# Optimization experiments

Hardware: AMD Instinct MI355X
Metric: run time of the kernel (lower is better)

The kernel has to match this reference:

```python
import jax, jax.numpy as jnp
import numpy as np

N, D, K = 262144, 64, 512


def setup_inputs() -> dict:
    key = jax.random.key(0)
    k1, k2 = jax.random.split(key)
    x = jax.random.normal(k1, (N, D), dtype=jnp.float32)
    # embedding initialized uniform(-1/K, 1/K) as in the torch module
    codebook = jax.random.uniform(k2, (K, D), dtype=jnp.float32, minval=-1.0 / K, maxval=1.0 / K)
    return {"x": x, "codebook": codebook}


def reference(x, codebook):
    # distances[n,k] = ||x_n||^2 + ||w_k||^2 - 2 x_n . w_k  (cdist^2 via matmul)
    d = (jnp.sum(x * x, axis=1, keepdims=True)
         + jnp.sum(codebook * codebook, axis=1)
         - 2.0 * jnp.matmul(x, codebook.T))  # [N, K]
    indices = jnp.argmin(d, axis=1)          # [N]
    x_q = codebook[indices]                  # [N, D] gather
    commitment_loss = jnp.mean((jax.lax.stop_gradient(x_q) - x) ** 2)
    embedding_loss = jnp.mean((x_q - jax.lax.stop_gradient(x)) ** 2)
    vq_loss = commitment_loss * 0.25 + embedding_loss
    # straight-through estimator
    x_out = x + jax.lax.stop_gradient(x_q - x)
    return (x_out, vq_loss)
```

## Files before the change

kernel.cpp:

```cpp
#include <hip/hip_runtime.h>
#include <hip/hip_bf16.h>

#define N_ROWS 262144
#define DIM    64
#define KCB    512

#define BLOCKS  512
#define THREADS 512

typedef __bf16 bf16x8 __attribute__((ext_vector_type(8)));
typedef float  f32x4  __attribute__((ext_vector_type(4)));

__device__ inline float dot4(float4 a) {
    return a.x * a.x + a.y * a.y + a.z * a.z + a.w * a.w;
}
__device__ inline unsigned umin2(unsigned a, unsigned b) { return a < b ? a : b; }

__device__ inline void conv_col(float4 f0, float4 f1, float4 f2, float4 f3,
                                bf16x8& lo, bf16x8& hi, float& xn) {
    xn = dot4(f0) + dot4(f1) + dot4(f2) + dot4(f3);
    lo[0] = (__bf16)f0.x; lo[1] = (__bf16)f0.y; lo[2] = (__bf16)f0.z; lo[3] = (__bf16)f0.w;
    lo[4] = (__bf16)f1.x; lo[5] = (__bf16)f1.y; lo[6] = (__bf16)f1.z; lo[7] = (__bf16)f1.w;
    hi[0] = (__bf16)f2.x; hi[1] = (__bf16)f2.y; hi[2] = (__bf16)f2.z; hi[3] = (__bf16)f2.w;
    hi[4] = (__bf16)f3.x; hi[5] = (__bf16)f3.y; hi[6] = (__bf16)f3.z; hi[7] = (__bf16)f3.w;
}

__global__ __launch_bounds__(THREADS, 2) void vq_main(
    const float* __restrict__ x, const float* __restrict__ cb,
    float* __restrict__ out, float* __restrict__ partials)
{
    __shared__ bf16x8 cb_sh[KCB * 8];
    __shared__ f32x4  wn_sh4[KCB / 4];
    __shared__ float  red_sh[8];

    const int tid    = threadIdx.x;
    const int lane   = tid & 63;
    const int wave   = tid >> 6;
    const int lane15 = lane & 15;
    const int half   = lane >> 4;

    const int wrow = blockIdx.x * 512 + wave * 64;
    const float* xc0 = x + (size_t)(wrow + lane15) * DIM + half * 8;
    const float* xc1 = x + (size_t)(wrow + 16 + lane15) * DIM + half * 8;

    float4 p00 = *(const float4*)xc0,        p01 = *(const float4*)(xc0 + 4);
    float4 p02 = *(const float4*)(xc0 + 32), p03 = *(const float4*)(xc0 + 36);
    float4 p10 = *(const float4*)xc1,        p11 = *(const float4*)(xc1 + 4);
    float4 p12 = *(const float4*)(xc1 + 32), p13 = *(const float4*)(xc1 + 36);

    #pragma unroll
    for (int it = 0; it < (KCB * 8) / THREADS; ++it) {
        const int fg = tid + it * THREADS;
        const int row = fg >> 3, g = fg & 7;
        const float* src = cb + row * DIM + g * 8;
        float4 f0 = *(const float4*)src;
        float4 f1 = *(const float4*)(src + 4);
        float sq = dot4(f0) + dot4(f1);
        sq += __shfl_xor(sq, 1);
        sq += __shfl_xor(sq, 2);
        sq += __shfl_xor(sq, 4);
        bf16x8 v;
        v[0] = (__bf16)(-f0.x); v[1] = (__bf16)(-f0.y); v[2] = (__bf16)(-f0.z); v[3] = (__bf16)(-f0.w);
        v[4] = (__bf16)(-f1.x); v[5] = (__bf16)(-f1.y); v[6] = (__bf16)(-f1.z); v[7] = (__bf16)(-f1.w);
        cb_sh[row * 8 + (g ^ (row & 7))] = v;
        if (g == 0) ((float*)wn_sh4)[row] = 1.0f + 0.5f * sq;
    }

    bf16x8 b0lo, b0hi, b1lo, b1hi;
    float  xn0, xn1;
    conv_col(p00, p01, p02, p03, b0lo, b0hi, xn0);
    conv_col(p10, p11, p12, p13, b1lo, b1hi, xn1);
    __syncthreads();

    float4 q00 = *(const float4*)(xc0 + 2048),  q01 = *(const float4*)(xc0 + 2052);
    float4 q02 = *(const float4*)(xc0 + 2080),  q03 = *(const float4*)(xc0 + 2084);
    float4 q10 = *(const float4*)(xc1 + 2048),  q11 = *(const float4*)(xc1 + 2052);
    float4 q12 = *(const float4*)(xc1 + 2080),  q13 = *(const float4*)(xc1 + 2084);

    const int swz_lo = half ^ (lane & 7);
    const int swz_hi = (4 + half) ^ (lane & 7);
    const unsigned hb = (unsigned)(half * 4);
    float lossAcc = 0.f;

    #pragma unroll
    for (int ch = 0; ch < 2; ++ch) {
        if (ch == 1) {
            conv_col(q00, q01, q02, q03, b0lo, b0hi, xn0);
            conv_col(q10, q11, q12, q13, b1lo, b1hi, xn1);
        }
        unsigned u0 = 0xFFFFFFFFu, u1 = 0xFFFFFFFFu;

        #pragma unroll 8
        for (int t = 0; t < 32; ++t) {
            const int arow = t * 16 + lane15;
            bf16x8 alo = cb_sh[arow * 8 + swz_lo];
            bf16x8 ahi = cb_sh[arow * 8 + swz_hi];
            f32x4  wnv = wn_sh4[t * 4 + half];
            const unsigned kb = (unsigned)(t * 16) | hb;

            f32x4 acc = wnv;
            acc = __builtin_amdgcn_mfma_f32_16x16x32_bf16(alo, b0lo, acc, 0, 0, 0);
            acc = __builtin_amdgcn_mfma_f32_16x16x32_bf16(ahi, b0hi, acc, 0, 0, 0);
            unsigned p0 = (__float_as_uint(acc[0]) & 0xFFFFFE00u) | kb;
            unsigned p1 = (__float_as_uint(acc[1]) & 0xFFFFFE00u) | (kb | 1u);
            unsigned p2 = (__float_as_uint(acc[2]) & 0xFFFFFE00u) | (kb | 2u);
            unsigned p3 = (__float_as_uint(acc[3]) & 0xFFFFFE00u) | (kb | 3u);
            u0 = umin2(u0, umin2(umin2(p0, p1), umin2(p2, p3)));

            f32x4 acd = wnv;
            acd = __builtin_amdgcn_mfma_f32_16x16x32_bf16(alo, b1lo, acd, 0, 0, 0);
            acd = __builtin_amdgcn_mfma_f32_16x16x32_bf16(ahi, b1hi, acd, 0, 0, 0);
            unsigned r0 = (__float_as_uint(acd[0]) & 0xFFFFFE00u) | kb;
            unsigned r1 = (__float_as_uint(acd[1]) & 0xFFFFFE00u) | (kb | 1u);
            unsigned r2 = (__float_as_uint(acd[2]) & 0xFFFFFE00u) | (kb | 2u);
            unsigned r3 = (__float_as_uint(acd[3]) & 0xFFFFFE00u) | (kb | 3u);
            u1 = umin2(u1, umin2(umin2(r0, r1), umin2(r2, r3)));
        }

        unsigned f0 = u0;
        f0 = umin2(f0, (unsigned)__shfl_xor((int)f0, 16));
        f0 = umin2(f0, (unsigned)__shfl_xor((int)f0, 32));
        unsigned f1 = u1;
        f1 = umin2(f1, (unsigned)__shfl_xor((int)f1, 16));
        f1 = umin2(f1, (unsigned)__shfl_xor((int)f1, 32));

        float xs0 = xn0;
        xs0 += __shfl_xor(xs0, 16); xs0 += __shfl_xor(xs0, 32);
        float xs1 = xn1;
        xs1 += __shfl_xor(xs1, 16); xs1 += __shfl_xor(xs1, 32);

        float s0 = __uint_as_float(f0 & 0xFFFFFE00u);
        float s1 = __uint_as_float(f1 & 0xFFFFFE00u);
        lossAcc += 0.25f * (xs0 + 2.f * (s0 - 1.f));
        lossAcc += 0.25f * (xs1 + 2.f * (s1 - 1.f));

        const int bk0 = (int)(f0 & 511u);
        const int bk1 = (int)(f1 & 511u);

        float* outw = out + (size_t)(wrow + ch * 32) * DIM;
        #pragma unroll
        for (int j = 0; j < 8; ++j) {
            const int srcl = (j * 4 + half) & 15;
            int bk = __shfl((j >> 2) ? bk1 : bk0, srcl);
            float4 qv = *(const float4*)(cb + (size_t)bk * DIM + (lane & 15) * 4);
            *(float4*)(outw + j * 256 + lane * 4) = qv;
        }
    }

    #pragma unroll
    for (int off = 1; off < 64; off <<= 1) lossAcc += __shfl_xor(lossAcc, off);
    if (lane == 0) red_sh[wave] = lossAcc;
    __syncthreads();
    if (tid == 0) {
        float s = 0.f;
        #pragma unroll
        for (int w = 0; w < 8; ++w) s += red_sh[w];
        partials[blockIdx.x] = s;
    }
}

__global__ void vq_finalize(const float* __restrict__ partials,
                            float* __restrict__ out_loss) {
    __shared__ float sh[256];
    int t = threadIdx.x;
    sh[t] = partials[t] + partials[t + 256];
    __syncthreads();
    #pragma unroll
    for (int s = 128; s > 0; s >>= 1) {
        if (t < s) sh[t] += sh[t + s];
        __syncthreads();
    }
    if (t == 0) out_loss[0] = sh[0] * (1.25f / (float)(N_ROWS * DIM));
}

extern "C" void kernel_launch(void* const* d_in, const int* in_sizes, int n_in,
                              void* d_out, int out_size, void* d_ws, size_t ws_size,
                              hipStream_t stream) {
    const float* x  = (const float*)d_in[0];
    const float* cb = (const float*)d_in[1];
    float* out      = (float*)d_out;
    float* partials = (float*)d_ws;

    hipLaunchKernelGGL(vq_main, dim3(BLOCKS), dim3(THREADS), 0, stream,
                       x, cb, out, partials);
    hipLaunchKernelGGL(vq_finalize, dim3(1), dim3(256), 0, stream,
                       partials, out + (size_t)N_ROWS * DIM);
}
```

Measured before the change: 39.96 us.

## Switch distance MFMA to FP8 and halve rows per block with more blocks

Replaces the bf16 codebook and x operands with scaled FP8 e4m3 packs and uses the fp8 16x16x32 MFMA. The codebook is scaled by -256 and the norm bias is rescaled to match, so that small codebook values fit in the fp8 range. Each block now handles 256 rows in a single pass instead of 512 rows in two chunks, with twice as many blocks and a higher occupancy hint. This removes the second-chunk prefetch, but the codebook must now be staged into LDS by twice as many blocks. FP8 quantization of x and the codebook risks argmin mismatches against the reference.

Result: slower. 45.97 us (+15.0%).

```diff
diff --git a/kernel.cpp b/kernel.cpp
--- a/kernel.cpp
+++ b/kernel.cpp
@@ -1,35 +1,40 @@
 #include <hip/hip_runtime.h>
 #include <hip/hip_bf16.h>
+#include <hip/hip_fp8.h>
 
 #define N_ROWS 262144
 #define DIM    64
 #define KCB    512
 
-#define BLOCKS  512
+#define BLOCKS  1024
 #define THREADS 512
 
-typedef __bf16 bf16x8 __attribute__((ext_vector_type(8)));
-typedef float  f32x4  __attribute__((ext_vector_type(4)));
+typedef float f32x4 __attribute__((ext_vector_type(4)));
 
 __device__ inline float dot4(float4 a) {
     return a.x * a.x + a.y * a.y + a.z * a.z + a.w * a.w;
 }
 __device__ inline unsigned umin2(unsigned a, unsigned b) { return a < b ? a : b; }
 
-__device__ inline void conv_col(float4 f0, float4 f1, float4 f2, float4 f3,
-                                bf16x8& lo, bf16x8& hi, float& xn) {
-    xn = dot4(f0) + dot4(f1) + dot4(f2) + dot4(f3);
-    lo[0] = (__bf16)f0.x; lo[1] = (__bf16)f0.y; lo[2] = (__bf16)f0.z; lo[3] = (__bf16)f0.w;
-    lo[4] = (__bf16)f1.x; lo[5] = (__bf16)f1.y; lo[6] = (__bf16)f1.z; lo[7] = (__bf16)f1.w;
-    hi[0] = (__bf16)f2.x; hi[1] = (__bf16)f2.y; hi[2] = (__bf16)f2.z; hi[3] = (__bf16)f2.w;
-    hi[4] = (__bf16)f3.x; hi[5] = (__bf16)f3.y; hi[6] = (__bf16)f3.z; hi[7] = (__bf16)f3.w;
+__device__ inline unsigned pk4(float a, float b, float c, float d) {
+    unsigned r;
+    r  = (unsigned)__hip_fp8_e4m3(a).__x;
+    r |= (unsigned)__hip_fp8_e4m3(b).__x << 8;
+    r |= (unsigned)__hip_fp8_e4m3(c).__x << 16;
+    r |= (unsigned)__hip_fp8_e4m3(d).__x << 24;
+    return r;
+}
+__device__ inline long pk8(float4 f0, float4 f1, float s) {
+    unsigned lo = pk4(f0.x * s, f0.y * s, f0.z * s, f0.w * s);
+    unsigned hi = pk4(f1.x * s, f1.y * s, f1.z * s, f1.w * s);
+    return (long)(((unsigned long)hi << 32) | (unsigned long)lo);
 }
 
-__global__ __launch_bounds__(THREADS, 2) void vq_main(
+__global__ __launch_bounds__(THREADS, 8) void vq_main(
     const float* __restrict__ x, const float* __restrict__ cb,
     float* __restrict__ out, float* __restrict__ partials)
 {
-    __shared__ bf16x8 cb_sh[KCB * 8];
+    __shared__ long   cb8_sh[KCB * 8];
     __shared__ f32x4  wn_sh4[KCB / 4];
     __shared__ float  red_sh[8];
 
@@ -39,7 +44,7 @@
     const int lane15 = lane & 15;
     const int half   = lane >> 4;
 
-    const int wrow = blockIdx.x * 512 + wave * 64;
+    const int wrow = blockIdx.x * 256 + wave * 32;
     const float* xc0 = x + (size_t)(wrow + lane15) * DIM + half * 8;
     const float* xc1 = x + (size_t)(wrow + 16 + lane15) * DIM + half * 8;
 
@@ -59,92 +64,76 @@
         sq += __shfl_xor(sq, 1);
         sq += __shfl_xor(sq, 2);
         sq += __shfl_xor(sq, 4);
-        bf16x8 v;
-        v[0] = (__bf16)(-f0.x); v[1] = (__bf16)(-f0.y); v[2] = (__bf16)(-f0.z); v[3] = (__bf16)(-f0.w);
-        v[4] = (__bf16)(-f1.x); v[5] = (__bf16)(-f1.y); v[6] = (__bf16)(-f1.z); v[7] = (__bf16)(-f1.w);
-        cb_sh[row * 8 + (g ^ (row & 7))] = v;
-        if (g == 0) ((float*)wn_sh4)[row] = 1.0f + 0.5f * sq;
+        cb8_sh[row * 8 + (g ^ (row & 7))] = pk8(f0, f1, -256.0f);
+        if (g == 0) ((float*)wn_sh4)[row] = 256.0f + 128.0f * sq;
     }
 
-    bf16x8 b0lo, b0hi, b1lo, b1hi;
-    float  xn0, xn1;
-    conv_col(p00, p01, p02, p03, b0lo, b0hi, xn0);
-    conv_col(p10, p11, p12, p13, b1lo, b1hi, xn1);
+    float xn0 = dot4(p00) + dot4(p01) + dot4(p02) + dot4(p03);
+    float xn1 = dot4(p10) + dot4(p11) + dot4(p12) + dot4(p13);
+    long b0lo = pk8(p00, p01, 1.0f), b0hi = pk8(p02, p03, 1.0f);
+    long b1lo = pk8(p10, p11, 1.0f), b1hi = pk8(p12, p13, 1.0f);
     __syncthreads();
-
-    float4 q00 = *(const float4*)(xc0 + 2048),  q01 = *(const float4*)(xc0 + 2052);
-    float4 q02 = *(const float4*)(xc0 + 2080),  q03 = *(const float4*)(xc0 + 2084);
-    float4 q10 = *(const float4*)(xc1 + 2048),  q11 = *(const float4*)(xc1 + 2052);
-    float4 q12 = *(const float4*)(xc1 + 2080),  q13 = *(const float4*)(xc1 + 2084);
 
     const int swz_lo = half ^ (lane & 7);
     const int swz_hi = (4 + half) ^ (lane & 7);
     const unsigned hb = (unsigned)(half * 4);
-    float lossAcc = 0.f;
 
+    unsigned u0 = 0xFFFFFFFFu, u1 = 0xFFFFFFFFu;
+
+    #pragma unroll 8
+    for (int t = 0; t < 32; ++t) {
+        const int arow = t * 16 + lane15;
+        long  alo = cb8_sh[arow * 8 + swz_lo];
+        long  ahi = cb8_sh[arow * 8 + swz_hi];
+        f32x4 wnv = wn_sh4[t * 4 + half];
+        const unsigned kb = (unsigned)(t * 16) | hb;
+
+        f32x4 acc = wnv;
+        acc = __builtin_amdgcn_mfma_f32_16x16x32_fp8_fp8(alo, b0lo, acc, 0, 0, 0);
+        acc = __builtin_amdgcn_mfma_f32_16x16x32_fp8_fp8(ahi, b0hi, acc, 0, 0, 0);
+        unsigned p0 = (__float_as_uint(acc[0]) & 0xFFFFFE00u) | kb;
+        unsigned p1 = (__float_as_uint(acc[1]) & 0xFFFFFE00u) | (kb | 1u);
+        unsigned p2 = (__float_as_uint(acc[2]) & 0xFFFFFE00u) | (kb | 2u);
+        unsigned p3 = (__float_as_uint(acc[3]) & 0xFFFFFE00u) | (kb | 3u);
+        u0 = umin2(u0, umin2(umin2(p0, p1), umin2(p2, p3)));
+
+        f32x4 acd = wnv;
+        acd = __builtin_amdgcn_mfma_f32_16x16x32_fp8_fp8(alo, b1lo, acd, 0, 0, 0);
+        acd = __builtin_amdgcn_mfma_f32_16x16x32_fp8_fp8(ahi, b1hi, acd, 0, 0, 0);
+        unsigned r0 = (__float_as_uint(acd[0]) & 0xFFFFFE00u) | kb;
+        unsigned r1 = (__float_as_uint(acd[1]) & 0xFFFFFE00u) | (kb | 1u);
+        unsigned r2 = (__float_as_uint(acd[2]) & 0xFFFFFE00u) | (kb | 2u);
+        unsigned r3 = (__float_as_uint(acd[3]) & 0xFFFFFE00u) | (kb | 3u);
+        u1 = umin2(u1, umin2(umin2(r0, r1), umin2(r2, r3)));
+    }
+
+    unsigned f0 = u0;
+    f0 = umin2(f0, (unsigned)__shfl_xor((int)f0, 16));
+    f0 = umin2(f0, (unsigned)__shfl_xor((int)f0, 32));
+    unsigned f1 = u1;
+    f1 = umin2(f1, (unsigned)__shfl_xor((int)f1, 16));
+    f1 = umin2(f1, (unsigned)__shfl_xor((int)f1, 32));
+
+    float xs0 = xn0;
+    xs0 += __shfl_xor(xs0, 16); xs0 += __shfl_xor(xs0, 32);
+    float xs1 = xn1;
+    xs1 += __shfl_xor(xs1, 16); xs1 += __shfl_xor(xs1, 32);
+
+    float pf0 = __uint_as_float(f0 & 0xFFFFFE00u);
+    float pf1 = __uint_as_float(f1 & 0xFFFFFE00u);
+    float lossAcc = 0.25f * (xs0 + pf0 * (1.0f / 128.0f) - 2.0f)
+                  + 0.25f * (xs1 + pf1 * (1.0f / 128.0f) - 2.0f);
+
+    const int bk0 = (int)(f0 & 511u);
+    const int bk1 = (int)(f1 & 511u);
+
+    float* outw = out + (size_t)wrow * DIM;
     #pragma unroll
-    for (int ch = 0; ch < 2; ++ch) {
-        if (ch == 1) {
-            conv_col(q00, q01, q02, q03, b0lo, b0hi, xn0);
-            conv_col(q10, q11, q12, q13, b1lo, b1hi, xn1);
-        }
-        unsigned u0 = 0xFFFFFFFFu, u1 = 0xFFFFFFFFu;
-
-        #pragma unroll 8
-        for (int t = 0; t < 32; ++t) {
-            const int arow = t * 16 + lane15;
-            bf16x8 alo = cb_sh[arow * 8 + swz_lo];
-            bf16x8 ahi = cb_sh[arow * 8 + swz_hi];
-            f32x4  wnv = wn_sh4[t * 4 + half];
-            const unsigned kb = (unsigned)(t * 16) | hb;
-
-            f32x4 acc = wnv;
-            acc = __builtin_amdgcn_mfma_f32_16x16x32_bf16(alo, b0lo, acc, 0, 0, 0);
-            acc = __builtin_amdgcn_mfma_f32_16x16x32_bf16(ahi, b0hi, acc, 0, 0, 0);
-            unsigned p0 = (__float_as_uint(acc[0]) & 0xFFFFFE00u) | kb;
-            unsigned p1 = (__float_as_uint(acc[1]) & 0xFFFFFE00u) | (kb | 1u);
-            unsigned p2 = (__float_as_uint(acc[2]) & 0xFFFFFE00u) | (kb | 2u);
-            unsigned p3 = (__float_as_uint(acc[3]) & 0xFFFFFE00u) | (kb | 3u);
-            u0 = umin2(u0, umin2(umin2(p0, p1), umin2(p2, p3)));
-
-            f32x4 acd = wnv;
-            acd = __builtin_amdgcn_mfma_f32_16x16x32_bf16(alo, b1lo, acd, 0, 0, 0);
-            acd = __builtin_amdgcn_mfma_f32_16x16x32_bf16(ahi, b1hi, acd, 0, 0, 0);
-            unsigned r0 = (__float_as_uint(acd[0]) & 0xFFFFFE00u) | kb;
-            unsigned r1 = (__float_as_uint(acd[1]) & 0xFFFFFE00u) | (kb | 1u);
-            unsigned r2 = (__float_as_uint(acd[2]) & 0xFFFFFE00u) | (kb | 2u);
-            unsigned r3 = (__float_as_uint(acd[3]) & 0xFFFFFE00u) | (kb | 3u);
-            u1 = umin2(u1, umin2(umin2(r0, r1), umin2(r2, r3)));
-        }
-
-        unsigned f0 = u0;
-        f0 = umin2(f0, (unsigned)__shfl_xor((int)f0, 16));
-        f0 = umin2(f0, (unsigned)__shfl_xor((int)f0, 32));
-        unsigned f1 = u1;
-        f1 = umin2(f1, (unsigned)__shfl_xor((int)f1, 16));
-        f1 = umin2(f1, (unsigned)__shfl_xor((int)f1, 32));
-
-        float xs0 = xn0;
-        xs0 += __shfl_xor(xs0, 16); xs0 += __shfl_xor(xs0, 32);
-        float xs1 = xn1;
-        xs1 += __shfl_xor(xs1, 16); xs1 += __shfl_xor(xs1, 32);
-
-        float s0 = __uint_as_float(f0 & 0xFFFFFE00u);
-        float s1 = __uint_as_float(f1 & 0xFFFFFE00u);
-        lossAcc += 0.25f * (xs0 + 2.f * (s0 - 1.f));
-        lossAcc += 0.25f * (xs1 + 2.f * (s1 - 1.f));
-
-        const int bk0 = (int)(f0 & 511u);
-        const int bk1 = (int)(f1 & 511u);
-
-        float* outw = out + (size_t)(wrow + ch * 32) * DIM;
-        #pragma unroll
-        for (int j = 0; j < 8; ++j) {
-            const int srcl = (j * 4 + half) & 15;
-            int bk = __shfl((j >> 2) ? bk1 : bk0, srcl);
-            float4 qv = *(const float4*)(cb + (size_t)bk * DIM + (lane & 15) * 4);
-            *(float4*)(outw + j * 256 + lane * 4) = qv;
-        }
+    for (int j = 0; j < 8; ++j) {
+        const int srcl = (j * 4 + half) & 15;
+        int bk = __shfl((j >> 2) ? bk1 : bk0, srcl);
+        float4 qv = *(const float4*)(cb + (size_t)bk * DIM + (lane & 15) * 4);
+        *(float4*)(outw + j * 256 + lane * 4) = qv;
     }
 
     #pragma unroll
@@ -163,7 +152,7 @@
                             float* __restrict__ out_loss) {
     __shared__ float sh[256];
     int t = threadIdx.x;
-    sh[t] = partials[t] + partials[t + 256];
+    sh[t] = partials[t] + partials[t + 256] + partials[t + 512] + partials[t + 768];
     __syncthreads();
     #pragma unroll
     for (int s = 128; s > 0; s >>= 1) {
```
